# Kernel optimization log

Measured on AMD Instinct MI355X. Metric: run time of the kernel, lower is better.

Reference implementation:

```python
import jax, jax.numpy as jnp
import numpy as np

N_ORB = 1024    # Monte-Carlo orbits
NTIMES = 1024   # observation epochs
N_FZ = 24       # zodi flux grid points (uniform in log10)
N_KEZ = 6       # exozodi multipliers (sorted, searchsorted lookup)
N_TINT = 64     # integration times
N_ALPHA = 512   # separations (uniform in log10)


def setup_inputs() -> dict:
    key = jax.random.key(0)
    k1, k2, k3, k4 = jax.random.split(key, 4)
    fZs = jnp.logspace(-10.0, -7.0, N_FZ).astype(jnp.float32)
    alphas = jnp.logspace(-2.0, 1.0, N_ALPHA).astype(jnp.float32)
    kEZs = jnp.array([0.5, 1.0, 2.0, 5.0, 10.0, 20.0], dtype=jnp.float32)
    # grid already in the module's internal (n_fZ, n_kEZ, n_tint, n_alpha) layout
    grid = 25.0 + jax.random.normal(k1, (N_FZ, N_KEZ, N_TINT, N_ALPHA), dtype=jnp.float32)
    # alpha slightly exceeds [alphas[0], alphas[-1]] so geom_mask is exercised
    alpha = (10.0 ** jax.random.uniform(k2, (N_ORB, NTIMES), minval=-2.2, maxval=1.1)).astype(jnp.float32)
    dMag = (25.0 + jax.random.normal(k3, (N_ORB, NTIMES))).astype(jnp.float32)
    fZ_vals = (10.0 ** jax.random.uniform(k4, (NTIMES,), minval=-10.0, maxval=-7.0)).astype(jnp.float32)
    kEZ_val = jnp.float32(1.5)
    return dict(alpha=alpha, dMag=dMag, fZ_vals=fZ_vals, kEZ_val=kEZ_val,
                grid=grid, fZs=fZs, kEZs=kEZs, alphas=alphas)


def reference(alpha, dMag, fZ_vals, kEZ_val, grid, fZs, kEZs, alphas):
    """Faithful vectorized translation of dMag0Grid._pdet_alpha_dMag.

    alpha, dMag: (n_orb, ntimes); fZ_vals: (ntimes,); kEZ_val: scalar;
    grid: (n_fZ, n_kEZ, n_tint, n_alpha). Returns pdet (ntimes, n_tint).
    """
    n_fZ = fZs.shape[0]
    n_alpha = alphas.shape[0]
    log_fZs = jnp.log10(fZs)
    inv_log_fZ_step = 1.0 / (log_fZs[1] - log_fZs[0])
    log_alphas = jnp.log10(alphas)
    inv_log_alpha_step = 1.0 / (log_alphas[1] - log_alphas[0])

    geom_mask = (alpha >= alphas[0]) & (alpha <= alphas[-1])          # (n_orb, ntimes)

    fZ_ind = (jnp.log10(fZ_vals) - log_fZs[0]) * inv_log_fZ_step
    fZ0 = jnp.clip(jnp.floor(fZ_ind).astype(jnp.int32) + 1, 0, n_fZ - 2)  # (ntimes,)

    a_ind = (jnp.log10(alpha) - log_alphas[0]) * inv_log_alpha_step
    a0 = jnp.clip(a_ind.astype(jnp.int32), 0, n_alpha - 1)               # (n_orb, ntimes)
    dalpha = (a_ind - a0).astype(grid.dtype)

    kEZ_ind = jnp.searchsorted(kEZs, kEZ_val, side='right') - 1

    # lax.dynamic_slice clamps the start so the width-2 window fits:
    s = jnp.minimum(a0, n_alpha - 2)                                     # (n_orb, ntimes)

    g = jnp.take(grid, kEZ_ind, axis=1)                                  # (n_fZ, n_tint, n_alpha)
    g_f = g[fZ0]                                                          # (ntimes, n_tint, n_alpha)
    sT = s.T                                                              # (ntimes, n_orb)
    g0 = jnp.take_along_axis(g_f, sT[:, None, :], axis=2)                 # (ntimes, n_tint, n_orb)
    g1 = jnp.take_along_axis(g_f, (sT + 1)[:, None, :], axis=2)
    res = g0 + dalpha.T[:, None, :] * (g1 - g0)                           # (ntimes, n_tint, n_orb)

    dim = jnp.transpose(res, (2, 0, 1))                                   # (n_orb, ntimes, n_tint)
    det_mask = geom_mask[..., None] & jnp.signbit(dMag[..., None] - dim)
    pdet = det_mask.astype(jnp.float32).mean(axis=0)                      # (ntimes, n_tint)
    return pdet
```

## Files before the change

kernel.cpp:

```cpp
#include <hip/hip_runtime.h>
#include <math.h>

#define N_ORB   1024
#define NTIMES  1024
#define N_FZ    24
#define N_KEZ   6
#define N_TINT  64
#define N_ALPHA 512

#define GT_BYTES (N_FZ * N_ALPHA * N_TINT * 4)

__global__ __launch_bounds__(256) void transpose_grid(
    const float* __restrict__ grid, const float* __restrict__ kEZs,
    const float* __restrict__ kEZ_val_p, float* __restrict__ gT)
{
    __shared__ float tile[64 * 65];

    float kv = kEZ_val_p[0];
    int cnt = 0;
#pragma unroll
    for (int i = 0; i < N_KEZ; ++i) cnt += (kEZs[i] <= kv) ? 1 : 0;
    int kez = cnt - 1;
    kez = kez < 0 ? 0 : (kez > N_KEZ - 1 ? N_KEZ - 1 : kez);

    int fz   = blockIdx.x;
    int sc   = blockIdx.y;
    int w    = threadIdx.x >> 6;
    int lane = threadIdx.x & 63;

    const float* gsrc = grid + ((size_t)fz * N_KEZ + kez) * N_TINT * N_ALPHA;

#pragma unroll
    for (int r = 0; r < 16; ++r) {
        int tint = w * 16 + r;
        tile[tint * 65 + lane] = gsrc[(size_t)tint * N_ALPHA + sc * 64 + lane];
    }
    __syncthreads();
#pragma unroll
    for (int r = 0; r < 16; ++r) {
        int sl = w * 16 + r;
        gT[((size_t)fz * N_ALPHA + sc * 64 + sl) * N_TINT + lane] = tile[lane * 65 + sl];
    }
}

__global__ __launch_bounds__(256) void prep_orbits(
    const float* __restrict__ alpha, const float* __restrict__ dMag,
    const float* __restrict__ alphas, float4* __restrict__ P)
{
    __shared__ float da_t[64 * 65];
    __shared__ float dm_t[64 * 65];
    __shared__ int   of_t[64 * 65];

    float al0 = alphas[0], al1 = alphas[N_ALPHA - 1];
    float la0 = log10f(al0);
    float inv_step = 1.0f / (log10f(alphas[1]) - la0);

    int o0 = blockIdx.y * 64, t0 = blockIdx.x * 64;
    int w = threadIdx.x >> 6, lane = threadIdx.x & 63;

#pragma unroll
    for (int r = 0; r < 16; ++r) {
        int ol = w * 16 + r;
        size_t idx = (size_t)(o0 + ol) * NTIMES + t0 + lane;
        float a = alpha[idx];
        float d = dMag[idx];
        float a_ind = (log10f(a) - la0) * inv_step;
        int a0i = (int)a_ind;
        a0i = a0i < 0 ? 0 : (a0i > N_ALPHA - 1 ? N_ALPHA - 1 : a0i);
        float dal = a_ind - (float)a0i;
        int s = a0i > N_ALPHA - 2 ? N_ALPHA - 2 : a0i;
        bool geom = (a >= al0) && (a <= al1);
        da_t[ol * 65 + lane] = dal;
        dm_t[ol * 65 + lane] = geom ? d : __builtin_inff();
        of_t[ol * 65 + lane] = s * N_TINT;
    }
    __syncthreads();
#pragma unroll
    for (int r = 0; r < 16; ++r) {
        int tl = w * 16 + r;
        float4 v;
        v.x = da_t[lane * 65 + tl];
        v.y = dm_t[lane * 65 + tl];
        v.z = __int_as_float(of_t[lane * 65 + tl]);
        v.w = 0.0f;
        P[(size_t)(t0 + tl) * N_ORB + o0 + lane] = v;
    }
}

__global__ __launch_bounds__(256) void pdet_main(
    const float* __restrict__ fZ_vals, const float* __restrict__ fZs,
    const float* __restrict__ gT, const float4* __restrict__ P,
    float* __restrict__ out)
{
    __shared__ float4 Psort[N_ORB];
    __shared__ int    hist[512];
    __shared__ int    histPS[512];
    __shared__ int    red[4 * 64];
    __shared__ int    aliveLDS;

    int t = blockIdx.x;
    int tid = threadIdx.x;
    int w = tid >> 6, lane = tid & 63;

    float lf0 = log10f(fZs[0]);
    float inv_f = 1.0f / (log10f(fZs[1]) - lf0);
    float fi = (log10f(fZ_vals[t]) - lf0) * inv_f;
    int f0 = (int)floorf(fi) + 1;
    f0 = f0 < 0 ? 0 : (f0 > N_FZ - 2 ? N_FZ - 2 : f0);

    const float*  gB = gT + (size_t)f0 * N_ALPHA * N_TINT;
    const float4* Pt = P + (size_t)t * N_ORB;

    hist[tid] = 0; hist[tid + 256] = 0;
    __syncthreads();

    float4 v[4];
    int    bin[4];
#pragma unroll
    for (int k = 0; k < 4; ++k) {
        v[k] = Pt[tid + k * 256];
        int s = __float_as_int(v[k].z) >> 6;
        bin[k] = isinf(v[k].y) ? 511 : s;
        atomicAdd(&hist[bin[k]], 1);
    }
    __syncthreads();

    if (tid < 64) {
        int pre[8]; int run = 0;
#pragma unroll
        for (int j = 0; j < 8; ++j) { pre[j] = run; run += hist[tid * 8 + j]; }
        int inc = run;
#pragma unroll
        for (int d = 1; d < 64; d <<= 1) {
            int n = __shfl_up(inc, d);
            if (lane >= d) inc += n;
        }
        int excl = inc - run;
#pragma unroll
        for (int j = 0; j < 8; ++j) histPS[tid * 8 + j] = excl + pre[j];
        if (tid == 63) aliveLDS = excl + pre[7] + hist[511] - hist[511];
        if (tid == 63) aliveLDS = excl + pre[7];
    }
    __syncthreads();

#pragma unroll
    for (int k = 0; k < 4; ++k) {
        int pos = atomicAdd(&histPS[bin[k]], 1);
        Psort[pos] = v[k];
    }
    __syncthreads();

    int alive = aliveLDS;
    int nIter = (alive + 15) >> 4;

    int q  = lane >> 4;
    int tg = (lane & 15) << 2;
    int sid = w * 4 + q;

    int c0 = 0, c1 = 0, c2 = 0, c3 = 0;

#pragma unroll 4
    for (int it = 0; it < nIter; ++it) {
        float4 pd = Psort[it * 16 + sid];
        float dal = pd.x, dm = pd.y;
        int offw = __float_as_int(pd.z);
        const float4* row = reinterpret_cast<const float4*>(gB + offw + tg);
        float4 g0 = row[0];
        float4 g1 = row[16];
        c0 += dm < fmaf(dal, g1.x - g0.x, g0.x);
        c1 += dm < fmaf(dal, g1.y - g0.y, g0.y);
        c2 += dm < fmaf(dal, g1.z - g0.z, g0.z);
        c3 += dm < fmaf(dal, g1.w - g0.w, g0.w);
    }

    c0 += __shfl_xor(c0, 16); c0 += __shfl_xor(c0, 32);
    c1 += __shfl_xor(c1, 16); c1 += __shfl_xor(c1, 32);
    c2 += __shfl_xor(c2, 16); c2 += __shfl_xor(c2, 32);
    c3 += __shfl_xor(c3, 16); c3 += __shfl_xor(c3, 32);

    if (lane < 16) {
        red[w * 64 + lane * 4 + 0] = c0;
        red[w * 64 + lane * 4 + 1] = c1;
        red[w * 64 + lane * 4 + 2] = c2;
        red[w * 64 + lane * 4 + 3] = c3;
    }
    __syncthreads();
    if (tid < 64) {
        int tot = red[tid] + red[64 + tid] + red[128 + tid] + red[192 + tid];
        out[(size_t)t * N_TINT + tid] = (float)tot * (1.0f / 1024.0f);
    }
}

extern "C" void kernel_launch(void* const* d_in, const int* in_sizes, int n_in,
                              void* d_out, int out_size, void* d_ws, size_t ws_size,
                              hipStream_t stream) {
    const float* alpha   = (const float*)d_in[0];
    const float* dMag    = (const float*)d_in[1];
    const float* fZ_vals = (const float*)d_in[2];
    const float* kEZ_val = (const float*)d_in[3];
    const float* grid    = (const float*)d_in[4];
    const float* fZs     = (const float*)d_in[5];
    const float* kEZs    = (const float*)d_in[6];
    const float* alphas  = (const float*)d_in[7];
    float*  out = (float*)d_out;

    float*  gT = (float*)d_ws;
    float4* P  = (float4*)((char*)d_ws + GT_BYTES);

    transpose_grid<<<dim3(N_FZ, N_ALPHA / 64), 256, 0, stream>>>(grid, kEZs, kEZ_val, gT);
    prep_orbits<<<dim3(NTIMES / 64, N_ORB / 64), 256, 0, stream>>>(alpha, dMag, alphas, P);
    pdet_main<<<dim3(NTIMES), 256, 0, stream>>>(fZ_vals, fZs, gT, P, out);
}
```

Before: 108.1 us.

## Fuse grid transpose and orbit prep into one launch, fixed per-wave orbit chunks

Merges the grid transpose and orbit preprocessing kernels into a single launch, using 32x32 tiles for the orbit prep. This removes one kernel launch and lets the two independent stages overlap. In the main kernel, the alive-count early exit is dropped and each wave instead processes a contiguous quarter of the sorted orbits for a fixed 64 iterations. That may improve grid-row locality and remove a dependent loop bound, but masked orbits are now processed too.

```diff
diff --git a/kernel.cpp b/kernel.cpp
--- a/kernel.cpp
+++ b/kernel.cpp
@@ -10,80 +10,78 @@
 
 #define GT_BYTES (N_FZ * N_ALPHA * N_TINT * 4)
 
-__global__ __launch_bounds__(256) void transpose_grid(
+__global__ __launch_bounds__(256) void stage_inputs(
     const float* __restrict__ grid, const float* __restrict__ kEZs,
-    const float* __restrict__ kEZ_val_p, float* __restrict__ gT)
+    const float* __restrict__ kEZ_val_p, const float* __restrict__ alpha,
+    const float* __restrict__ dMag, const float* __restrict__ alphas,
+    float* __restrict__ gT, float4* __restrict__ P)
 {
-    __shared__ float tile[64 * 65];
-
-    float kv = kEZ_val_p[0];
-    int cnt = 0;
-#pragma unroll
-    for (int i = 0; i < N_KEZ; ++i) cnt += (kEZs[i] <= kv) ? 1 : 0;
-    int kez = cnt - 1;
-    kez = kez < 0 ? 0 : (kez > N_KEZ - 1 ? N_KEZ - 1 : kez);
-
-    int fz   = blockIdx.x;
-    int sc   = blockIdx.y;
-    int w    = threadIdx.x >> 6;
-    int lane = threadIdx.x & 63;
-
-    const float* gsrc = grid + ((size_t)fz * N_KEZ + kez) * N_TINT * N_ALPHA;
-
-#pragma unroll
-    for (int r = 0; r < 16; ++r) {
-        int tint = w * 16 + r;
-        tile[tint * 65 + lane] = gsrc[(size_t)tint * N_ALPHA + sc * 64 + lane];
-    }
-    __syncthreads();
-#pragma unroll
-    for (int r = 0; r < 16; ++r) {
-        int sl = w * 16 + r;
-        gT[((size_t)fz * N_ALPHA + sc * 64 + sl) * N_TINT + lane] = tile[lane * 65 + sl];
-    }
-}
-
-__global__ __launch_bounds__(256) void prep_orbits(
-    const float* __restrict__ alpha, const float* __restrict__ dMag,
-    const float* __restrict__ alphas, float4* __restrict__ P)
-{
-    __shared__ float da_t[64 * 65];
-    __shared__ float dm_t[64 * 65];
-    __shared__ int   of_t[64 * 65];
-
-    float al0 = alphas[0], al1 = alphas[N_ALPHA - 1];
-    float la0 = log10f(al0);
-    float inv_step = 1.0f / (log10f(alphas[1]) - la0);
-
-    int o0 = blockIdx.y * 64, t0 = blockIdx.x * 64;
-    int w = threadIdx.x >> 6, lane = threadIdx.x & 63;
-
-#pragma unroll
-    for (int r = 0; r < 16; ++r) {
-        int ol = w * 16 + r;
-        size_t idx = (size_t)(o0 + ol) * NTIMES + t0 + lane;
-        float a = alpha[idx];
-        float d = dMag[idx];
-        float a_ind = (log10f(a) - la0) * inv_step;
-        int a0i = (int)a_ind;
-        a0i = a0i < 0 ? 0 : (a0i > N_ALPHA - 1 ? N_ALPHA - 1 : a0i);
-        float dal = a_ind - (float)a0i;
-        int s = a0i > N_ALPHA - 2 ? N_ALPHA - 2 : a0i;
-        bool geom = (a >= al0) && (a <= al1);
-        da_t[ol * 65 + lane] = dal;
-        dm_t[ol * 65 + lane] = geom ? d : __builtin_inff();
-        of_t[ol * 65 + lane] = s * N_TINT;
-    }
-    __syncthreads();
-#pragma unroll
-    for (int r = 0; r < 16; ++r) {
-        int tl = w * 16 + r;
-        float4 v;
-        v.x = da_t[lane * 65 + tl];
-        v.y = dm_t[lane * 65 + tl];
-        v.z = __int_as_float(of_t[lane * 65 + tl]);
-        v.w = 0.0f;
-        P[(size_t)(t0 + tl) * N_ORB + o0 + lane] = v;
+    __shared__ float lds[64 * 65];
+
+    int b = blockIdx.x;
+    if (b < 192) {
+        float kv = kEZ_val_p[0];
+        int cnt = 0;
+#pragma unroll
+        for (int i = 0; i < N_KEZ; ++i) cnt += (kEZs[i] <= kv) ? 1 : 0;
+        int kez = cnt - 1;
+        kez = kez < 0 ? 0 : (kez > N_KEZ - 1 ? N_KEZ - 1 : kez);
+
+        int fz = b >> 3, sc = b & 7;
+        int w = threadIdx.x >> 6, lane = threadIdx.x & 63;
+        const float* gsrc = grid + ((size_t)fz * N_KEZ + kez) * N_TINT * N_ALPHA;
+
+#pragma unroll
+        for (int r = 0; r < 16; ++r) {
+            int tint = w * 16 + r;
+            lds[tint * 65 + lane] = gsrc[(size_t)tint * N_ALPHA + sc * 64 + lane];
+        }
+        __syncthreads();
+#pragma unroll
+        for (int r = 0; r < 16; ++r) {
+            int sl = w * 16 + r;
+            gT[((size_t)fz * N_ALPHA + sc * 64 + sl) * N_TINT + lane] = lds[lane * 65 + sl];
+        }
+    } else {
+        float* da = lds;
+        float* dm = lds + 1056;
+        int*   of = (int*)(lds + 2112);
+
+        int u = b - 192;
+        int t0 = (u & 31) * 32, o0 = (u >> 5) * 32;
+        int row = threadIdx.x >> 5, col = threadIdx.x & 31;
+
+        float al0 = alphas[0], al1 = alphas[N_ALPHA - 1];
+        float la0 = log10f(al0);
+        float inv_step = 1.0f / (log10f(alphas[1]) - la0);
+
+#pragma unroll
+        for (int r = 0; r < 4; ++r) {
+            int ol = r * 8 + row;
+            size_t idx = (size_t)(o0 + ol) * NTIMES + t0 + col;
+            float a = alpha[idx];
+            float d = dMag[idx];
+            float a_ind = (log10f(a) - la0) * inv_step;
+            int a0i = (int)a_ind;
+            a0i = a0i < 0 ? 0 : (a0i > N_ALPHA - 1 ? N_ALPHA - 1 : a0i);
+            float dal = a_ind - (float)a0i;
+            int s = a0i > N_ALPHA - 2 ? N_ALPHA - 2 : a0i;
+            bool geom = (a >= al0) && (a <= al1);
+            da[ol * 33 + col] = dal;
+            dm[ol * 33 + col] = geom ? d : __builtin_inff();
+            of[ol * 33 + col] = s * N_TINT;
+        }
+        __syncthreads();
+#pragma unroll
+        for (int r = 0; r < 4; ++r) {
+            int tl = r * 8 + row;
+            float4 v;
+            v.x = da[col * 33 + tl];
+            v.y = dm[col * 33 + tl];
+            v.z = __int_as_float(of[col * 33 + tl]);
+            v.w = 0.0f;
+            P[(size_t)(t0 + tl) * N_ORB + o0 + col] = v;
+        }
     }
 }
 
@@ -96,7 +94,6 @@
     __shared__ int    hist[512];
     __shared__ int    histPS[512];
     __shared__ int    red[4 * 64];
-    __shared__ int    aliveLDS;
 
     int t = blockIdx.x;
     int tid = threadIdx.x;
@@ -138,8 +135,6 @@
         int excl = inc - run;
 #pragma unroll
         for (int j = 0; j < 8; ++j) histPS[tid * 8 + j] = excl + pre[j];
-        if (tid == 63) aliveLDS = excl + pre[7] + hist[511] - hist[511];
-        if (tid == 63) aliveLDS = excl + pre[7];
     }
     __syncthreads();
 
@@ -150,23 +145,20 @@
     }
     __syncthreads();
 
-    int alive = aliveLDS;
-    int nIter = (alive + 15) >> 4;
-
     int q  = lane >> 4;
     int tg = (lane & 15) << 2;
-    int sid = w * 4 + q;
+    int base = w * 256;
 
     int c0 = 0, c1 = 0, c2 = 0, c3 = 0;
 
 #pragma unroll 4
-    for (int it = 0; it < nIter; ++it) {
-        float4 pd = Psort[it * 16 + sid];
+    for (int it = 0; it < 64; ++it) {
+        float4 pd = Psort[base + it * 4 + q];
         float dal = pd.x, dm = pd.y;
         int offw = __float_as_int(pd.z);
-        const float4* row = reinterpret_cast<const float4*>(gB + offw + tg);
-        float4 g0 = row[0];
-        float4 g1 = row[16];
+        const float4* rowp = reinterpret_cast<const float4*>(gB + offw + tg);
+        float4 g0 = rowp[0];
+        float4 g1 = rowp[16];
         c0 += dm < fmaf(dal, g1.x - g0.x, g0.x);
         c1 += dm < fmaf(dal, g1.y - g0.y, g0.y);
         c2 += dm < fmaf(dal, g1.z - g0.z, g0.z);
@@ -207,7 +199,7 @@
     float*  gT = (float*)d_ws;
     float4* P  = (float4*)((char*)d_ws + GT_BYTES);
 
-    transpose_grid<<<dim3(N_FZ, N_ALPHA / 64), 256, 0, stream>>>(grid, kEZs, kEZ_val, gT);
-    prep_orbits<<<dim3(NTIMES / 64, N_ORB / 64), 256, 0, stream>>>(alpha, dMag, alphas, P);
+    stage_inputs<<<dim3(192 + 1024), 256, 0, stream>>>(
+        grid, kEZs, kEZ_val, alpha, dMag, alphas, gT, P);
     pdet_main<<<dim3(NTIMES), 256, 0, stream>>>(fZ_vals, fZs, gT, P, out);
 }
```

Measured after the change: 104.2 us. 3.6% less time.
